# Kernel tuning notes

Hardware: AMD Instinct MI355X
Metric: run time of the kernel (lower is better)

The kernel has to match this reference:

```python
import math
import jax, jax.numpy as jnp
import numpy as np

L, D, H, F, V, S, B = 6, 1024, 16, 4096, 32000, 1024, 2
DH = D // H


def setup_inputs() -> dict:
    key = jax.random.key(0)
    ks = jax.random.split(key, 24)

    def u(k, shape, fan_in):
        b = 1.0 / math.sqrt(fan_in)
        return jax.random.uniform(k, shape, jnp.float32, -b, b)

    inp = {
        "input_ids": jax.random.randint(ks[0], (B, S), 0, V),
        "attention_mask": jnp.ones((B, 1, 1, S), dtype=bool),
        "emb": jax.random.normal(ks[1], (V, D), jnp.float32),
        "pos": 0.02 * jax.random.normal(ks[2], (1, S, D), jnp.float32),
        "ln1_w": jnp.ones((L, D), jnp.float32),
        "ln1_b": jnp.zeros((L, D), jnp.float32),
        "qw": u(ks[3], (L, D, D), D), "qb": u(ks[4], (L, D), D),
        "kw": u(ks[5], (L, D, D), D), "kb": u(ks[6], (L, D), D),
        "vw": u(ks[7], (L, D, D), D), "vb": u(ks[8], (L, D), D),
        "ow": u(ks[9], (L, D, D), D), "ob": u(ks[10], (L, D), D),
        "ln2_w": jnp.ones((L, D), jnp.float32),
        "ln2_b": jnp.zeros((L, D), jnp.float32),
        "w1": u(ks[11], (L, F, D), D), "b1": u(ks[12], (L, F), D),
        "w2": u(ks[13], (L, D, F), F), "b2": u(ks[14], (L, D), F),
    }
    return inp


def _ln(x, w, b, eps=1e-5):
    m = x.mean(axis=-1, keepdims=True)
    v = ((x - m) ** 2).mean(axis=-1, keepdims=True)  # unbiased=False
    return w * (x - m) / jnp.sqrt(v + eps) + b


def _gelu(x):
    # tanh-approx GELU, exactly as in source
    return 0.5 * x * (1.0 + jnp.tanh(math.sqrt(2.0 / math.pi) * (x + 0.044715 * x ** 3)))


def reference(input_ids, attention_mask, emb, pos, ln1_w, ln1_b,
              qw, qb, kw, kb, vw, vb, ow, ob,
              ln2_w, ln2_b, w1, b1, w2, b2):
    b, s = input_ids.shape
    d = emb.shape[1]
    scale = math.sqrt(DH)
    x = emb[input_ids] * math.sqrt(d) + pos[:, :s, :]  # [B,S,D]
    n_layers = qw.shape[0]
    for l in range(n_layers):
        h = _ln(x, ln1_w[l], ln1_b[l])
        q = (h @ qw[l].T + qb[l]).reshape(b, s, H, DH)
        k = (h @ kw[l].T + kb[l]).reshape(b, s, H, DH)
        v = (h @ vw[l].T + vb[l]).reshape(b, s, H, DH)
        scores = jnp.einsum('bqhd,bkhd->bhqk', q, k) / scale  # [B,H,S,S]
        scores = jnp.where(attention_mask, scores, -jnp.inf)
        attn = jax.nn.softmax(scores, axis=-1)
        o = jnp.einsum('bhqk,bkhd->bqhd', attn, v).reshape(b, s, d)
        x = x + (o @ ow[l].T + ob[l])
        h2 = _ln(x, ln2_w[l], ln2_b[l])
        x = x + (_gelu(h2 @ w1[l].T + b1[l]) @ w2[l].T + b2[l])
    return x
```

## Files before the change

### kernel.cpp

```cpp
#include <hip/hip_runtime.h>
#include <hip/hip_bf16.h>
#include <math.h>

#define D_ 1024
#define H_ 16
#define F_ 4096
#define S_ 1024
#define B_ 2
#define MTOT 2048

using bf16 = __hip_bfloat16;
typedef __bf16 bf16x8 __attribute__((ext_vector_type(8)));
typedef float f32x4 __attribute__((ext_vector_type(4)));

__device__ __forceinline__ void gload_lds16(const void* g, void* l) {
  __builtin_amdgcn_global_load_lds((const __attribute__((address_space(1))) void*)g,
                                   (__attribute__((address_space(3))) void*)l, 16, 0, 0);
}

__device__ __forceinline__ unsigned short f2b(float f) {
  union { bf16 h; unsigned short u; } c;
  c.h = __float2bfloat16(f);
  return c.u;
}

__device__ __forceinline__ unsigned pk2(float a, float b) {
  return (unsigned)f2b(a) | ((unsigned)f2b(b) << 16);
}

__global__ __launch_bounds__(256) void embed_kernel(const int* __restrict__ ids,
    const float* __restrict__ emb, const float* __restrict__ pos, float* __restrict__ x) {
  int row = blockIdx.x;
  int s = row & (S_ - 1);
  int id = ids[row];
  const float4* e = (const float4*)(emb + (size_t)id * D_);
  const float4* p = (const float4*)(pos + (size_t)s * D_);
  float4* xo = (float4*)(x + (size_t)row * D_);
  int t = threadIdx.x;
  float4 ev = e[t], pv = p[t], r;
  r.x = ev.x * 32.0f + pv.x; r.y = ev.y * 32.0f + pv.y;
  r.z = ev.z * 32.0f + pv.z; r.w = ev.w * 32.0f + pv.w;
  xo[t] = r;
}

__global__ __launch_bounds__(256) void ln_kernel(const float* __restrict__ x,
    const float* __restrict__ w, const float* __restrict__ b, bf16* __restrict__ h) {
  int row = blockIdx.x, t = threadIdx.x;
  const float4* xr = (const float4*)(x + (size_t)row * D_);
  float4 v = xr[t];
  float s = v.x + v.y + v.z + v.w;
  float s2 = v.x * v.x + v.y * v.y + v.z * v.z + v.w * v.w;
  #pragma unroll
  for (int o = 32; o; o >>= 1) { s += __shfl_down(s, o); s2 += __shfl_down(s2, o); }
  __shared__ float red[8];
  int wave = t >> 6, lane = t & 63;
  if (lane == 0) { red[wave] = s; red[4 + wave] = s2; }
  __syncthreads();
  float mean = (red[0] + red[1] + red[2] + red[3]) * (1.0f / D_);
  float m2   = (red[4] + red[5] + red[6] + red[7]) * (1.0f / D_);
  float rstd = rsqrtf(m2 - mean * mean + 1e-5f);
  float4 wv = ((const float4*)w)[t], bv = ((const float4*)b)[t];
  ushort4 o4;
  o4.x = f2b((v.x - mean) * rstd * wv.x + bv.x);
  o4.y = f2b((v.y - mean) * rstd * wv.y + bv.y);
  o4.z = f2b((v.z - mean) * rstd * wv.z + bv.z);
  o4.w = f2b((v.w - mean) * rstd * wv.w + bv.w);
  ((ushort4*)(h + (size_t)row * D_))[t] = o4;
}

template<int LSHIFT>
__global__ __launch_bounds__(256) void cvt_copy_kernel(const float4* __restrict__ src,
    ushort4* __restrict__ dst, int n4, int wl4) {
  int stride = gridDim.x * 256;
  for (int i = blockIdx.x * 256 + threadIdx.x; i < n4; i += stride) {
    int layer = i >> LSHIFT;
    int r = i & ((1 << LSHIFT) - 1);
    float4 v = src[i];
    ushort4 p;
    p.x = f2b(v.x); p.y = f2b(v.y); p.z = f2b(v.z); p.w = f2b(v.w);
    dst[(size_t)layer * wl4 + r] = p;
  }
}

template<int MODE>
__global__ __launch_bounds__(256) void gemm_bt(const bf16* __restrict__ A,
    const bf16* __restrict__ Bw,
    const float* __restrict__ b0_, const float* __restrict__ b1_, const float* __restrict__ b2_,
    void* __restrict__ o0, void* __restrict__ o1, void* __restrict__ o2,
    int M, int N, int K, int kspl) {
  __shared__ alignas(16) bf16 As[2][128 * 64];
  __shared__ alignas(16) bf16 Bs[2][128 * 64];
  int tid = threadIdx.x, wave = tid >> 6, lane = tid & 63;
  int nbn = N >> 7;
  int nwg = gridDim.x;
  int bid = blockIdx.x;
  int swz = (bid & 7) * (nwg >> 3) + (bid >> 3);
  int bm = swz / nbn, bn = swz % nbn;
  int m0 = bm << 7, n0 = bn << 7;
  int kbase = blockIdx.z * kspl;
  int wr = wave >> 1, wc = wave & 1;
  int lr = lane & 15, lg = lane >> 4;

  auto stage = [&](int buf, int k0) {
    #pragma unroll
    for (int j = 0; j < 4; j++) {
      int cidx = j * 256 + tid;
      int r = cidx >> 3, s = cidx & 7;
      int g = s ^ (r & 7);
      bf16* abase = &As[buf][(j * 256 + wave * 64) * 8];
      bf16* bbase = &Bs[buf][(j * 256 + wave * 64) * 8];
      gload_lds16(A  + (size_t)(m0 + r) * K + k0 + g * 8, abase);
      gload_lds16(Bw + (size_t)(n0 + r) * K + k0 + g * 8, bbase);
    }
  };

  f32x4 acc[4][4] = {};
  int nk = kspl >> 6;
  stage(0, kbase);
  __syncthreads();
  int cur = 0;
  for (int t = 0; t < nk; ++t) {
    if (t + 1 < nk) stage(cur ^ 1, kbase + (t + 1) * 64);
    __builtin_amdgcn_s_setprio(1);
    #pragma unroll
    for (int kk = 0; kk < 2; ++kk) {
      bf16x8 af[4], bfr[4];
      #pragma unroll
      for (int f = 0; f < 4; f++) {
        int ra = wr * 64 + f * 16 + lr;
        int rb = wc * 64 + f * 16 + lr;
        af[f]  = *(const bf16x8*)&As[cur][ra * 64 + (((kk * 4 + lg) ^ (ra & 7)) * 8)];
        bfr[f] = *(const bf16x8*)&Bs[cur][rb * 64 + (((kk * 4 + lg) ^ (rb & 7)) * 8)];
      }
      #pragma unroll
      for (int mf = 0; mf < 4; mf++)
        #pragma unroll
        for (int nf = 0; nf < 4; nf++)
          acc[mf][nf] = __builtin_amdgcn_mfma_f32_16x16x32_bf16(af[mf], bfr[nf], acc[mf][nf], 0, 0, 0);
    }
    __builtin_amdgcn_s_setprio(0);
    __syncthreads();
    cur ^= 1;
  }

  #pragma unroll
  for (int mf = 0; mf < 4; mf++) {
    #pragma unroll
    for (int nf = 0; nf < 4; nf++) {
      int n = n0 + wc * 64 + nf * 16 + lr;
      if (MODE == 0 && n >= 2048) {
        int nl = n & 1023;
        int mbase = m0 + wr * 64 + mf * 16 + lg * 4;
        int bb = mbase >> 10, sb = mbase & 1023;
        float bias = b2_[nl];
        ushort4 pk;
        pk.x = f2b(acc[mf][nf][0] + bias);
        pk.y = f2b(acc[mf][nf][1] + bias);
        pk.z = f2b(acc[mf][nf][2] + bias);
        pk.w = f2b(acc[mf][nf][3] + bias);
        *(ushort4*)&((bf16*)o2)[((size_t)(bb * 1024 + nl)) * 1024 + sb] = pk;
      } else {
        #pragma unroll
        for (int i = 0; i < 4; i++) {
          int m = m0 + wr * 64 + mf * 16 + lg * 4 + i;
          float v = acc[mf][nf][i];
          if (MODE == 0) {
            int seg = n >> 10, nl = n & 1023;
            if (seg == 0)      ((bf16*)o0)[(size_t)m * 1024 + nl] = __float2bfloat16(v + b0_[nl]);
            else               ((bf16*)o1)[(size_t)m * 1024 + nl] = __float2bfloat16(v + b1_[nl]);
          } else if (MODE == 1) {
            float bias = (blockIdx.z == 0) ? b0_[n] : 0.0f;
            atomicAdd(&((float*)o0)[(size_t)m * N + n], v + bias);
          } else {
            float g = v + b0_[n];
            float e = __expf(-1.5957691216057308f * (g + 0.044715f * g * g * g));
            ((bf16*)o0)[(size_t)m * N + n] = __float2bfloat16(g / (1.0f + e));
          }
        }
      }
    }
  }
}

__global__ __launch_bounds__(256) void attn_kernel(const bf16* __restrict__ qbuf,
    const bf16* __restrict__ kbuf, const bf16* __restrict__ vT, bf16* __restrict__ obuf) {
  int bh = blockIdx.y;
  int b = bh >> 4, h = bh & 15;
  int qblk = blockIdx.x * 64;
  int tid = threadIdx.x, wave = tid >> 6, lane = tid & 63;
  int lr = lane & 15, lg = lane >> 4;

  __shared__ alignas(16) bf16 Ks[2][32 * 64];
  __shared__ alignas(16) bf16 Vs[2][64 * 32];

  auto stage = [&](int buf, int c) {
    int kb = c * 32;
    {
      int r = tid >> 3, s = tid & 7, g = s ^ (r & 7);
      gload_lds16(kbuf + (size_t)(b * S_ + kb + r) * D_ + h * 64 + g * 8,
                  &Ks[buf][wave * 512]);
    }
    {
      int d = tid >> 2, s = tid & 3, g = s ^ (d & 3);
      gload_lds16(vT + (size_t)(b * D_ + h * 64 + d) * S_ + kb + g * 8,
                  &Vs[buf][wave * 512]);
    }
  };

  const bf16* qp = qbuf + (size_t)(b * S_ + qblk + wave * 16 + lr) * D_ + h * 64;
  bf16x8 qf0 = *(const bf16x8*)(qp + lg * 8);
  bf16x8 qf1 = *(const bf16x8*)(qp + 32 + lg * 8);

  f32x4 oacc[4] = {};
  float m_run = -1e30f, l_run = 0.0f;
  int x7 = lr & 7, x3 = lr & 3;

  stage(0, 0);
  __syncthreads();
  int cur = 0;
  for (int c = 0; c < 32; ++c) {
    if (c + 1 < 32) stage(cur ^ 1, c + 1);

    bf16x8 ka00 = *(const bf16x8*)&Ks[cur][lr * 64 + ((lg ^ x7) * 8)];
    bf16x8 ka01 = *(const bf16x8*)&Ks[cur][lr * 64 + (((4 + lg) ^ x7) * 8)];
    bf16x8 ka10 = *(const bf16x8*)&Ks[cur][(16 + lr) * 64 + ((lg ^ x7) * 8)];
    bf16x8 ka11 = *(const bf16x8*)&Ks[cur][(16 + lr) * 64 + (((4 + lg) ^ x7) * 8)];
    f32x4 sa = {}, sb = {};
    sa = __builtin_amdgcn_mfma_f32_16x16x32_bf16(ka00, qf0, sa, 0, 0, 0);
    sa = __builtin_amdgcn_mfma_f32_16x16x32_bf16(ka01, qf1, sa, 0, 0, 0);
    sb = __builtin_amdgcn_mfma_f32_16x16x32_bf16(ka10, qf0, sb, 0, 0, 0);
    sb = __builtin_amdgcn_mfma_f32_16x16x32_bf16(ka11, qf1, sb, 0, 0, 0);

    float p[8];
    #pragma unroll
    for (int i = 0; i < 4; i++) { p[i] = sa[i] * 0.125f; p[4 + i] = sb[i] * 0.125f; }
    float cmax = p[0];
    #pragma unroll
    for (int j = 1; j < 8; j++) cmax = fmaxf(cmax, p[j]);
    cmax = fmaxf(cmax, __shfl_xor(cmax, 16));
    cmax = fmaxf(cmax, __shfl_xor(cmax, 32));
    float m_new = fmaxf(m_run, cmax);
    float fsc = __expf(m_run - m_new);
    m_run = m_new;
    float csum = 0.0f;
    #pragma unroll
    for (int j = 0; j < 8; j++) { p[j] = __expf(p[j] - m_new); csum += p[j]; }
    csum += __shfl_xor(csum, 16);
    csum += __shfl_xor(csum, 32);
    l_run = l_run * fsc + csum;

    float f0 = __shfl(fsc, lg * 4 + 0);
    float f1 = __shfl(fsc, lg * 4 + 1);
    float f2 = __shfl(fsc, lg * 4 + 2);
    float f3 = __shfl(fsc, lg * 4 + 3);
    #pragma unroll
    for (int nf = 0; nf < 4; nf++) {
      oacc[nf][0] *= f0; oacc[nf][1] *= f1; oacc[nf][2] *= f2; oacc[nf][3] *= f3;
    }

    unsigned A0 = pk2(p[0], p[1]), A1 = pk2(p[2], p[3]);
    unsigned B0 = pk2(p[4], p[5]), B1 = pk2(p[6], p[7]);
    int slo = 32 * (lg & 1) + lr, shi = slo + 16;
    unsigned tA0 = __shfl(A0, slo), tB0 = __shfl(B0, slo);
    unsigned tA1 = __shfl(A1, slo), tB1 = __shfl(B1, slo);
    unsigned uA0 = __shfl(A0, shi), uB0 = __shfl(B0, shi);
    unsigned uA1 = __shfl(A1, shi), uB1 = __shfl(B1, shi);
    bool loh = (lg < 2);
    union { unsigned w[4]; bf16x8 v; } pfu;
    pfu.w[0] = loh ? tA0 : tB0;
    pfu.w[1] = loh ? tA1 : tB1;
    pfu.w[2] = loh ? uA0 : uB0;
    pfu.w[3] = loh ? uA1 : uB1;
    bf16x8 pf = pfu.v;

    #pragma unroll
    for (int nf = 0; nf < 4; nf++) {
      bf16x8 vf = *(const bf16x8*)&Vs[cur][(nf * 16 + lr) * 32 + ((lg ^ x3) * 8)];
      oacc[nf] = __builtin_amdgcn_mfma_f32_16x16x32_bf16(pf, vf, oacc[nf], 0, 0, 0);
    }

    __syncthreads();
    cur ^= 1;
  }

  float l0 = __shfl(l_run, lg * 4 + 0);
  float l1 = __shfl(l_run, lg * 4 + 1);
  float l2 = __shfl(l_run, lg * 4 + 2);
  float l3 = __shfl(l_run, lg * 4 + 3);
  float li[4] = {l0, l1, l2, l3};
  #pragma unroll
  for (int i = 0; i < 4; i++) {
    size_t row = (size_t)(b * S_ + qblk + wave * 16 + lg * 4 + i) * D_ + h * 64;
    #pragma unroll
    for (int nf = 0; nf < 4; nf++)
      obuf[row + nf * 16 + lr] = __float2bfloat16(oacc[nf][i] / li[i]);
  }
}

extern "C" void kernel_launch(void* const* d_in, const int* in_sizes, int n_in,
                              void* d_out, int out_size, void* d_ws, size_t ws_size,
                              hipStream_t stream) {
  const int*   ids  = (const int*)d_in[0];
  const float* emb  = (const float*)d_in[2];
  const float* pos  = (const float*)d_in[3];
  const float* ln1w = (const float*)d_in[4];
  const float* ln1b = (const float*)d_in[5];
  const float* qw = (const float*)d_in[6];  const float* qb = (const float*)d_in[7];
  const float* kw = (const float*)d_in[8];  const float* kb = (const float*)d_in[9];
  const float* vw = (const float*)d_in[10]; const float* vb = (const float*)d_in[11];
  const float* ow = (const float*)d_in[12]; const float* ob = (const float*)d_in[13];
  const float* ln2w = (const float*)d_in[14]; const float* ln2b = (const float*)d_in[15];
  const float* w1 = (const float*)d_in[16]; const float* b1 = (const float*)d_in[17];
  const float* w2 = (const float*)d_in[18]; const float* b2 = (const float*)d_in[19];
  (void)in_sizes; (void)n_in; (void)out_size; (void)ws_size;

  float* x = (float*)d_out;
  char* ws = (char*)d_ws;
  const size_t SZ_ACT = (size_t)MTOT * D_ * 2;
  bf16* h    = (bf16*)(ws);
  bf16* q    = (bf16*)(ws + SZ_ACT);
  bf16* k    = (bf16*)(ws + 2 * SZ_ACT);
  bf16* vt   = (bf16*)(ws + 3 * SZ_ACT);
  bf16* o    = (bf16*)(ws + 4 * SZ_ACT);
  bf16* mid  = (bf16*)(ws + 5 * SZ_ACT);
  bf16* wbuf = (bf16*)(ws + 5 * SZ_ACT + (size_t)MTOT * F_ * 2);

  const size_t DD = (size_t)D_ * D_;
  const size_t FD = (size_t)F_ * D_;
  const size_t WL = 4 * DD + 2 * FD;

  const int WL4 = (int)(WL / 4);
  cvt_copy_kernel<18><<<2048, 256, 0, stream>>>((const float4*)qw,
      (ushort4*)(wbuf + 0 * DD), (int)(6 * DD / 4), WL4);
  cvt_copy_kernel<18><<<2048, 256, 0, stream>>>((const float4*)kw,
      (ushort4*)(wbuf + 1 * DD), (int)(6 * DD / 4), WL4);
  cvt_copy_kernel<18><<<2048, 256, 0, stream>>>((const float4*)vw,
      (ushort4*)(wbuf + 2 * DD), (int)(6 * DD / 4), WL4);
  cvt_copy_kernel<18><<<2048, 256, 0, stream>>>((const float4*)ow,
      (ushort4*)(wbuf + 3 * DD), (int)(6 * DD / 4), WL4);
  cvt_copy_kernel<20><<<2048, 256, 0, stream>>>((const float4*)w1,
      (ushort4*)(wbuf + 4 * DD), (int)(6 * FD / 4), WL4);
  cvt_copy_kernel<20><<<2048, 256, 0, stream>>>((const float4*)w2,
      (ushort4*)(wbuf + 4 * DD + FD), (int)(6 * FD / 4), WL4);

  embed_kernel<<<MTOT, 256, 0, stream>>>(ids, emb, pos, x);

  for (int l = 0; l < 6; l++) {
    bf16* wl = wbuf + (size_t)l * WL;

    ln_kernel<<<MTOT, 256, 0, stream>>>(x, ln1w + l * D_, ln1b + l * D_, h);

    gemm_bt<0><<<dim3(384, 1, 1), 256, 0, stream>>>(h, wl,
        qb + l * D_, kb + l * D_, vb + l * D_, q, k, vt, MTOT, 3072, 1024, 1024);

    attn_kernel<<<dim3(16, 32), 256, 0, stream>>>(q, k, vt, o);

    gemm_bt<1><<<dim3(128, 1, 2), 256, 0, stream>>>(o, wl + 3 * DD,
        ob + l * D_, nullptr, nullptr, x, nullptr, nullptr, MTOT, 1024, 1024, 512);

    ln_kernel<<<MTOT, 256, 0, stream>>>(x, ln2w + l * D_, ln2b + l * D_, h);

    gemm_bt<2><<<dim3(512, 1, 1), 256, 0, stream>>>(h, wl + 4 * DD,
        b1 + l * F_, nullptr, nullptr, mid, nullptr, nullptr, MTOT, 4096, 1024, 1024);

    gemm_bt<1><<<dim3(128, 1, 2), 256, 0, stream>>>(mid, wl + 4 * DD + FD,
        b2 + l * D_, nullptr, nullptr, x, nullptr, nullptr, MTOT, 1024, 4096, 2048);
  }
}
```

Measured before the change: 1.123 ms.

## Double attention KV chunk size and skip softmax rescale when max barely grows

The flash-attention loop now stages 64 keys per iteration instead of 32, halving the iteration count and the barriers per head. The V tile swizzle and the MFMA sequence are reworked to match. It also adds a lazy online-softmax rescale: the running max and the accumulator rescale are only updated when some row's chunk max exceeds the running max by more than 8. This saves exp and multiply work on most iterations, at the cost of doubled LDS use and unnormalised exponents that can reach about e^8, which is still safe in fp32 and bf16.

```diff
diff --git a/kernel.cpp b/kernel.cpp
--- a/kernel.cpp
+++ b/kernel.cpp
@@ -190,20 +190,24 @@
   int tid = threadIdx.x, wave = tid >> 6, lane = tid & 63;
   int lr = lane & 15, lg = lane >> 4;
 
-  __shared__ alignas(16) bf16 Ks[2][32 * 64];
-  __shared__ alignas(16) bf16 Vs[2][64 * 32];
+  __shared__ alignas(16) bf16 Ks[2][64 * 64];
+  __shared__ alignas(16) bf16 Vs[2][64 * 64];
 
   auto stage = [&](int buf, int c) {
-    int kb = c * 32;
-    {
-      int r = tid >> 3, s = tid & 7, g = s ^ (r & 7);
+    int kb = c * 64;
+    #pragma unroll
+    for (int j = 0; j < 2; j++) {
+      int cidx = j * 256 + tid;
+      int r = cidx >> 3, s = cidx & 7, g = s ^ (r & 7);
       gload_lds16(kbuf + (size_t)(b * S_ + kb + r) * D_ + h * 64 + g * 8,
-                  &Ks[buf][wave * 512]);
-    }
-    {
-      int d = tid >> 2, s = tid & 3, g = s ^ (d & 3);
-      gload_lds16(vT + (size_t)(b * D_ + h * 64 + d) * S_ + kb + g * 8,
-                  &Vs[buf][wave * 512]);
+                  &Ks[buf][(j * 256 + wave * 64) * 8]);
+    }
+    #pragma unroll
+    for (int j = 0; j < 2; j++) {
+      int cidx = j * 256 + tid;
+      int r = cidx >> 3, s = cidx & 7, g = s ^ (r & 7);
+      gload_lds16(vT + (size_t)(b * D_ + h * 64 + r) * S_ + kb + g * 8,
+                  &Vs[buf][(j * 256 + wave * 64) * 8]);
     }
   };
 
@@ -213,70 +217,83 @@
 
   f32x4 oacc[4] = {};
   float m_run = -1e30f, l_run = 0.0f;
-  int x7 = lr & 7, x3 = lr & 3;
+  int x7 = lr & 7;
 
   stage(0, 0);
   __syncthreads();
   int cur = 0;
-  for (int c = 0; c < 32; ++c) {
-    if (c + 1 < 32) stage(cur ^ 1, c + 1);
-
-    bf16x8 ka00 = *(const bf16x8*)&Ks[cur][lr * 64 + ((lg ^ x7) * 8)];
-    bf16x8 ka01 = *(const bf16x8*)&Ks[cur][lr * 64 + (((4 + lg) ^ x7) * 8)];
-    bf16x8 ka10 = *(const bf16x8*)&Ks[cur][(16 + lr) * 64 + ((lg ^ x7) * 8)];
-    bf16x8 ka11 = *(const bf16x8*)&Ks[cur][(16 + lr) * 64 + (((4 + lg) ^ x7) * 8)];
-    f32x4 sa = {}, sb = {};
-    sa = __builtin_amdgcn_mfma_f32_16x16x32_bf16(ka00, qf0, sa, 0, 0, 0);
-    sa = __builtin_amdgcn_mfma_f32_16x16x32_bf16(ka01, qf1, sa, 0, 0, 0);
-    sb = __builtin_amdgcn_mfma_f32_16x16x32_bf16(ka10, qf0, sb, 0, 0, 0);
-    sb = __builtin_amdgcn_mfma_f32_16x16x32_bf16(ka11, qf1, sb, 0, 0, 0);
-
-    float p[8];
-    #pragma unroll
-    for (int i = 0; i < 4; i++) { p[i] = sa[i] * 0.125f; p[4 + i] = sb[i] * 0.125f; }
+  for (int c = 0; c < 16; ++c) {
+    if (c + 1 < 16) stage(cur ^ 1, c + 1);
+
+    float p[16];
+    #pragma unroll
+    for (int kg = 0; kg < 4; kg++) {
+      int row = kg * 16 + lr;
+      bf16x8 k0 = *(const bf16x8*)&Ks[cur][row * 64 + ((lg ^ x7) * 8)];
+      bf16x8 k1 = *(const bf16x8*)&Ks[cur][row * 64 + (((4 + lg) ^ x7) * 8)];
+      f32x4 s = {};
+      s = __builtin_amdgcn_mfma_f32_16x16x32_bf16(k0, qf0, s, 0, 0, 0);
+      s = __builtin_amdgcn_mfma_f32_16x16x32_bf16(k1, qf1, s, 0, 0, 0);
+      #pragma unroll
+      for (int i = 0; i < 4; i++) p[kg * 4 + i] = s[i] * 0.125f;
+    }
+
     float cmax = p[0];
     #pragma unroll
-    for (int j = 1; j < 8; j++) cmax = fmaxf(cmax, p[j]);
+    for (int j = 1; j < 16; j++) cmax = fmaxf(cmax, p[j]);
     cmax = fmaxf(cmax, __shfl_xor(cmax, 16));
     cmax = fmaxf(cmax, __shfl_xor(cmax, 32));
-    float m_new = fmaxf(m_run, cmax);
-    float fsc = __expf(m_run - m_new);
-    m_run = m_new;
+
+    if (__any(cmax > m_run + 8.0f)) {
+      float m_new = fmaxf(m_run, cmax);
+      float fsc = __expf(m_run - m_new);
+      m_run = m_new;
+      float f0 = __shfl(fsc, lg * 4 + 0);
+      float f1 = __shfl(fsc, lg * 4 + 1);
+      float f2 = __shfl(fsc, lg * 4 + 2);
+      float f3 = __shfl(fsc, lg * 4 + 3);
+      #pragma unroll
+      for (int nf = 0; nf < 4; nf++) {
+        oacc[nf][0] *= f0; oacc[nf][1] *= f1; oacc[nf][2] *= f2; oacc[nf][3] *= f3;
+      }
+      l_run *= fsc;
+    }
+
     float csum = 0.0f;
     #pragma unroll
-    for (int j = 0; j < 8; j++) { p[j] = __expf(p[j] - m_new); csum += p[j]; }
+    for (int j = 0; j < 16; j++) { p[j] = __expf(p[j] - m_run); csum += p[j]; }
     csum += __shfl_xor(csum, 16);
     csum += __shfl_xor(csum, 32);
-    l_run = l_run * fsc + csum;
-
-    float f0 = __shfl(fsc, lg * 4 + 0);
-    float f1 = __shfl(fsc, lg * 4 + 1);
-    float f2 = __shfl(fsc, lg * 4 + 2);
-    float f3 = __shfl(fsc, lg * 4 + 3);
+    l_run += csum;
+
+    bf16x8 pf[2];
+    int slo = 32 * (lg & 1) + lr, shi = slo + 16;
+    bool loh = (lg < 2);
+    #pragma unroll
+    for (int ks = 0; ks < 2; ks++) {
+      unsigned A0 = pk2(p[ks * 8 + 0], p[ks * 8 + 1]);
+      unsigned A1 = pk2(p[ks * 8 + 2], p[ks * 8 + 3]);
+      unsigned B0 = pk2(p[ks * 8 + 4], p[ks * 8 + 5]);
+      unsigned B1 = pk2(p[ks * 8 + 6], p[ks * 8 + 7]);
+      unsigned tA0 = __shfl(A0, slo), tB0 = __shfl(B0, slo);
+      unsigned tA1 = __shfl(A1, slo), tB1 = __shfl(B1, slo);
+      unsigned uA0 = __shfl(A0, shi), uB0 = __shfl(B0, shi);
+      unsigned uA1 = __shfl(A1, shi), uB1 = __shfl(B1, shi);
+      union { unsigned w[4]; bf16x8 v; } pfu;
+      pfu.w[0] = loh ? tA0 : tB0;
+      pfu.w[1] = loh ? tA1 : tB1;
+      pfu.w[2] = loh ? uA0 : uB0;
+      pfu.w[3] = loh ? uA1 : uB1;
+      pf[ks] = pfu.v;
+    }
+
     #pragma unroll
     for (int nf = 0; nf < 4; nf++) {
-      oacc[nf][0] *= f0; oacc[nf][1] *= f1; oacc[nf][2] *= f2; oacc[nf][3] *= f3;
-    }
-
-    unsigned A0 = pk2(p[0], p[1]), A1 = pk2(p[2], p[3]);
-    unsigned B0 = pk2(p[4], p[5]), B1 = pk2(p[6], p[7]);
-    int slo = 32 * (lg & 1) + lr, shi = slo + 16;
-    unsigned tA0 = __shfl(A0, slo), tB0 = __shfl(B0, slo);
-    unsigned tA1 = __shfl(A1, slo), tB1 = __shfl(B1, slo);
-    unsigned uA0 = __shfl(A0, shi), uB0 = __shfl(B0, shi);
-    unsigned uA1 = __shfl(A1, shi), uB1 = __shfl(B1, shi);
-    bool loh = (lg < 2);
-    union { unsigned w[4]; bf16x8 v; } pfu;
-    pfu.w[0] = loh ? tA0 : tB0;
-    pfu.w[1] = loh ? tA1 : tB1;
-    pfu.w[2] = loh ? uA0 : uB0;
-    pfu.w[3] = loh ? uA1 : uB1;
-    bf16x8 pf = pfu.v;
-
-    #pragma unroll
-    for (int nf = 0; nf < 4; nf++) {
-      bf16x8 vf = *(const bf16x8*)&Vs[cur][(nf * 16 + lr) * 32 + ((lg ^ x3) * 8)];
-      oacc[nf] = __builtin_amdgcn_mfma_f32_16x16x32_bf16(pf, vf, oacc[nf], 0, 0, 0);
+      int rv = nf * 16 + lr;
+      bf16x8 v0 = *(const bf16x8*)&Vs[cur][rv * 64 + ((lg ^ (rv & 7)) * 8)];
+      bf16x8 v1 = *(const bf16x8*)&Vs[cur][rv * 64 + (((4 + lg) ^ (rv & 7)) * 8)];
+      oacc[nf] = __builtin_amdgcn_mfma_f32_16x16x32_bf16(pf[0], v0, oacc[nf], 0, 0, 0);
+      oacc[nf] = __builtin_amdgcn_mfma_f32_16x16x32_bf16(pf[1], v1, oacc[nf], 0, 0, 0);
     }
 
     __syncthreads();
```

Result: faster. 1.056 ms (-6.0%).
